# Optimization experiments

Measured on AMD Instinct MI355X. Metric: run time of the kernel, lower is better.

Reference implementation:

```python
import jax, jax.numpy as jnp
import numpy as np

B, N, DIM = 1, 2048, 2048
H, KVH = 32, 4                 # query heads, kv heads
D = DIM // H                   # head_dim = 64
REP = H // KVH                 # queries per kv = 8
KV_DIM = D * KVH               # 256


def _rope_tables(n, d, base=10000.0):
    inv = 1.0 / (base ** (np.arange(0, d, 2, dtype=np.float32) / d))
    t = np.arange(n, dtype=np.float32)
    freqs = np.outer(t, inv)                      # [n, d/2]
    emb = np.concatenate([freqs, freqs], axis=-1)  # [n, d]
    return jnp.asarray(np.cos(emb)), jnp.asarray(np.sin(emb))


def setup_inputs() -> dict:
    key = jax.random.key(0)
    ks = jax.random.split(key, 5)
    s = 0.02
    cos, sin = _rope_tables(N, D)
    return {
        "x": jax.random.normal(ks[0], (B, N, DIM), jnp.float32),
        "Wq": jax.random.normal(ks[1], (DIM, DIM), jnp.float32) * s,
        "Wk": jax.random.normal(ks[2], (KV_DIM, DIM), jnp.float32) * s,
        "Wv": jax.random.normal(ks[3], (KV_DIM, DIM), jnp.float32) * s,
        "Wo": jax.random.normal(ks[4], (DIM, DIM), jnp.float32) * s,
        "cos": cos,
        "sin": sin,
    }


def _rotate_half(t):
    d2 = t.shape[-1] // 2
    return jnp.concatenate([-t[..., d2:], t[..., :d2]], axis=-1)


def reference(x, Wq, Wk, Wv, Wo, cos, sin):
    b, n, _ = x.shape
    # projections (nn.Linear: x @ W.T)
    q = (x @ Wq.T).reshape(b, n, H, D).transpose(0, 2, 1, 3)     # b h n d
    k = (x @ Wk.T).reshape(b, n, KVH, D).transpose(0, 2, 1, 3)   # b g n d
    v = (x @ Wv.T).reshape(b, n, KVH, D).transpose(0, 2, 1, 3)
    # RoPE
    c = cos[None, None, :, :]
    s = sin[None, None, :, :]
    q = q * c + _rotate_half(q) * s
    k = k * c + _rotate_half(k) * s
    # expand KV heads (repeat_interleave over head dim)
    k = jnp.repeat(k, REP, axis=1)   # b h n d
    v = jnp.repeat(v, REP, axis=1)
    # causal attention with materialized scores (faithful to source)
    scale = 1.0 / jnp.sqrt(jnp.asarray(D, x.dtype))
    scores = jnp.einsum('bhld,bhsd->bhls', q, k) * scale
    causal = jnp.tril(jnp.ones((n, n), bool))
    scores = jnp.where(causal[None, None], scores, jnp.asarray(-jnp.inf, x.dtype))
    attn = jax.nn.softmax(scores, axis=-1)
    y = jnp.einsum('bhls,bhsd->bhld', attn, v)       # b h n d
    y = y.transpose(0, 2, 1, 3).reshape(b, n, DIM)   # b n (h d)
    return y @ Wo.T
```

## Files before the change

### kernel.cpp

```cpp
#include <hip/hip_runtime.h>

typedef unsigned short u16;
typedef __attribute__((ext_vector_type(8))) short short8;
typedef __attribute__((ext_vector_type(4))) float floatx4;

#define N_TOK 2048
#define DIM   2048
#define NH    32
#define NKVH  4
#define HD    64
#define KVD   256

__device__ __forceinline__ float bf2f(u16 u) {
  union { unsigned i; float f; } c; c.i = ((unsigned)u) << 16; return c.f;
}
__device__ __forceinline__ u16 f2bf(float f) {
  union { float f; unsigned i; } c; c.f = f;
  unsigned x = c.i;
  return (u16)((x + 0x7fffu + ((x >> 16) & 1u)) >> 16);
}

__device__ __forceinline__ void gload16(const u16* g, u16* l) {
#if defined(__has_builtin) && __has_builtin(__builtin_amdgcn_global_load_lds)
  __builtin_amdgcn_global_load_lds(
      (const __attribute__((address_space(1))) void*)g,
      (__attribute__((address_space(3))) void*)l, 16, 0, 0);
#else
  *(short8*)l = *(const short8*)g;
#endif
}

#define C_X  1048576
#define C_WQ 2097152
#define C_WK 2228224
#define C_WV 2359296
#define C_WO 3407872
__global__ __launch_bounds__(256) void cvt_all(const float* __restrict__ x,
                                               const float* __restrict__ wq,
                                               const float* __restrict__ wk,
                                               const float* __restrict__ wv,
                                               const float* __restrict__ wo,
                                               u16* __restrict__ dst) {
  int i = blockIdx.x * 256 + threadIdx.x;
  const float* src; int off;
  if      (i < C_X)  { src = x;  off = 0; }
  else if (i < C_WQ) { src = wq; off = C_X; }
  else if (i < C_WK) { src = wk; off = C_WQ; }
  else if (i < C_WV) { src = wv; off = C_WK; }
  else               { src = wo; off = C_WV; }
  float4 v = ((const float4*)src)[i - off];
  ushort4 o;
  o.x = f2bf(v.x); o.y = f2bf(v.y); o.z = f2bf(v.z); o.w = f2bf(v.w);
  ((ushort4*)dst)[i] = o;
}


__global__ __launch_bounds__(256) void gemm_qkv(const u16* __restrict__ A,
                                                const u16* __restrict__ Wq,
                                                const u16* __restrict__ Wk,
                                                const u16* __restrict__ Wv,
                                                const float* __restrict__ cs,
                                                const float* __restrict__ sn,
                                                u16* __restrict__ Qp,
                                                u16* __restrict__ Kp,
                                                u16* __restrict__ Vp) {
  __shared__ __align__(16) u16 As[64 * 32];
  __shared__ __align__(16) u16 Bs[128 * 32];
  const int tid  = threadIdx.x;
  const int lane = tid & 63;
  const int w    = tid >> 6;
  const int r    = lane & 15, q = lane >> 4;
  const int tm = blockIdx.x & 31;
  const int tn = blockIdx.x >> 5;
  const int wm = w & 1, wn = w >> 1;
  const int K = DIM;

  const u16* W; int wrow0;
  if (tn < 16)      { W = Wq; wrow0 = tn * 128; }
  else if (tn < 18) { W = Wk; wrow0 = (tn - 16) * 128; }
  else              { W = Wv; wrow0 = (tn - 18) * 128; }

  const int srow = tid >> 2;
  const int scol = (tid & 3) * 8;
  const u16* ga = A + (size_t)(tm * 64 + srow) * K + scol;
  const u16* gb = W + (size_t)(wrow0 + srow) * K + scol;
  u16* lA = &As[tid * 8];
  u16* lB = &Bs[tid * 8];

  floatx4 acc[2][4];
#pragma unroll
  for (int a = 0; a < 2; ++a)
#pragma unroll
    for (int b = 0; b < 4; ++b) acc[a][b] = (floatx4){0.f, 0.f, 0.f, 0.f};

  for (int k0 = 0; k0 < K; k0 += 32) {
    __syncthreads();
    gload16(ga + k0, lA);
    gload16(gb + k0, lB);
    gload16(gb + k0 + (size_t)64 * K, lB + 2048);
    __syncthreads();

    short8 af[2], bf[4];
#pragma unroll
    for (int mi = 0; mi < 2; ++mi)
      af[mi] = *(const short8*)&As[(wm * 32 + mi * 16 + r) * 32 + q * 8];
#pragma unroll
    for (int nj = 0; nj < 4; ++nj)
      bf[nj] = *(const short8*)&Bs[(wn * 64 + nj * 16 + r) * 32 + q * 8];
#pragma unroll
    for (int mi = 0; mi < 2; ++mi)
#pragma unroll
      for (int nj = 0; nj < 4; ++nj)
        acc[mi][nj] = __builtin_amdgcn_mfma_f32_16x16x32_bf16(af[mi], bf[nj], acc[mi][nj], 0, 0, 0);
  }

  if (tn < 18) {
    const int head = (tn < 16) ? (tn * 2 + wn) : ((tn - 16) * 2 + wn);
#pragma unroll
    for (int mi = 0; mi < 2; ++mi)
#pragma unroll
      for (int g = 0; g < 4; ++g) {
        int row = tm * 64 + wm * 32 + mi * 16 + 4 * q + g;
        const float* crow  = cs + (size_t)row * 64;
        const float* srow2 = sn + (size_t)row * 64;
#pragma unroll
        for (int nj = 0; nj < 2; ++nj) {
          int d = nj * 16 + r;
          float x0 = acc[mi][nj][g];
          float x1 = acc[mi][nj + 2][g];
          float o0 = x0 * crow[d]      - x1 * srow2[d];
          float o1 = x1 * crow[d + 32] + x0 * srow2[d + 32];
          int qq = d >> 3, j = d & 7;
          int lslot = (qq * 16 + (row & 15)) * 8 + j;
          if (tn < 16) {
            int sq = row >> 5, ii = (row >> 4) & 1;
            size_t base = ((size_t)(head * 64 + sq) * 4 + ii * 2) * 512 + lslot;
            Qp[base]       = f2bf(o0);
            Qp[base + 512] = f2bf(o1);
          } else {
            int kt = row >> 6, t = (row >> 4) & 3;
            size_t base = ((size_t)(head * 32 + kt) * 8 + t * 2) * 512 + lslot;
            Kp[base]       = f2bf(o0);
            Kp[base + 512] = f2bf(o1);
          }
        }
      }
  } else {
#pragma unroll
    for (int mi = 0; mi < 2; ++mi)
#pragma unroll
      for (int nj = 0; nj < 4; ++nj) {
        int col  = (tn - 18) * 128 + wn * 64 + nj * 16 + r;
        int kvh  = col >> 6;
        int t    = (col & 63) >> 4;
        int rr   = col & 15;
        int row0 = tm * 64 + wm * 32 + mi * 16 + 4 * q;
        int kt   = row0 >> 6;
        int wk   = row0 & 63;
        int s    = wk >> 5;
        int qq   = (wk & 31) >> 3;
        int j0   = wk & 7;
        uint2 pk;
        pk.x = (unsigned)f2bf(acc[mi][nj][0]) | ((unsigned)f2bf(acc[mi][nj][1]) << 16);
        pk.y = (unsigned)f2bf(acc[mi][nj][2]) | ((unsigned)f2bf(acc[mi][nj][3]) << 16);
        size_t idx = ((size_t)(kvh * 32 + kt) * 8 + s * 4 + t) * 512 + (qq * 16 + rr) * 8 + j0;
        *(uint2*)(Vp + idx) = pk;
      }
  }
}

__global__ __launch_bounds__(256) void gemm_out(const u16* __restrict__ A,
                                                const u16* __restrict__ W,
                                                float* __restrict__ C) {
  __shared__ __align__(16) u16 As[64 * 32];
  __shared__ __align__(16) u16 Bs[128 * 32];
  const int tid  = threadIdx.x;
  const int lane = tid & 63;
  const int w    = tid >> 6;
  const int r    = lane & 15, q = lane >> 4;
  const int tn = blockIdx.x & 15;
  const int tm = blockIdx.x >> 4;
  const int wm = w & 1, wn = w >> 1;
  const int K = DIM;

  const int srow = tid >> 2;
  const int scol = (tid & 3) * 8;
  const u16* ga = A + (size_t)(tm * 64 + srow) * K + scol;
  const u16* gb = W + (size_t)(tn * 128 + srow) * K + scol;
  u16* lA = &As[tid * 8];
  u16* lB = &Bs[tid * 8];

  floatx4 acc[2][4];
#pragma unroll
  for (int a = 0; a < 2; ++a)
#pragma unroll
    for (int b = 0; b < 4; ++b) acc[a][b] = (floatx4){0.f, 0.f, 0.f, 0.f};

  for (int k0 = 0; k0 < K; k0 += 32) {
    __syncthreads();
    gload16(ga + k0, lA);
    gload16(gb + k0, lB);
    gload16(gb + k0 + (size_t)64 * K, lB + 2048);
    __syncthreads();

    short8 af[2], bf[4];
#pragma unroll
    for (int mi = 0; mi < 2; ++mi)
      af[mi] = *(const short8*)&As[(wm * 32 + mi * 16 + r) * 32 + q * 8];
#pragma unroll
    for (int nj = 0; nj < 4; ++nj)
      bf[nj] = *(const short8*)&Bs[(wn * 64 + nj * 16 + r) * 32 + q * 8];
#pragma unroll
    for (int mi = 0; mi < 2; ++mi)
#pragma unroll
      for (int nj = 0; nj < 4; ++nj)
        acc[mi][nj] = __builtin_amdgcn_mfma_f32_16x16x32_bf16(af[mi], bf[nj], acc[mi][nj], 0, 0, 0);
  }

#pragma unroll
  for (int mi = 0; mi < 2; ++mi)
#pragma unroll
    for (int g = 0; g < 4; ++g) {
      int row = tm * 64 + wm * 32 + mi * 16 + 4 * q + g;
#pragma unroll
      for (int nj = 0; nj < 4; ++nj)
        C[(size_t)row * DIM + tn * 128 + wn * 64 + nj * 16 + r] = acc[mi][nj][g];
    }
}

__global__ __launch_bounds__(128, 2) void attn_mfma(const u16* __restrict__ Qp,
                                                    const u16* __restrict__ Kp,
                                                    const u16* __restrict__ Vp,
                                                    u16* __restrict__ Yb) {
  __shared__ __align__(16) u16 Pl[2][32][72];
  __shared__ float OcA[32][66];
  __shared__ float OcB[32][66];
  __shared__ float LcA[2][64], LcB[2][64];
  const int tid  = threadIdx.x;
  const int lane = tid & 63;
  const int w    = tid >> 6;
  const int r    = lane & 15;
  const int q    = lane >> 4;
  const int p    = blockIdx.x;
  const int h    = blockIdx.y;
  const int kvh  = h >> 3;
  const int jA   = 63 - p;
  const int jB   = p;
  const int baseqA = jA * 32, baseqB = jB * 32;
  const int tA = (jA >> 1) + 1, tB = (jB >> 1) + 1;
  const int ktmaxA = tA - 1, ktmaxB = tB - 1;

  short8 qfA[2][2], qfB[2][2];
#pragma unroll
  for (int i = 0; i < 2; ++i)
#pragma unroll
    for (int c = 0; c < 2; ++c) {
      qfA[i][c] = *(const short8*)(Qp + ((size_t)(h * 64 + jA) * 4 + i * 2 + c) * 512 + lane * 8);
      qfB[i][c] = *(const short8*)(Qp + ((size_t)(h * 64 + jB) * 4 + i * 2 + c) * 512 + lane * 8);
    }

  floatx4 OA[2][4], OB[2][4];
  float lsumA[2], lsumB[2];
#pragma unroll
  for (int i = 0; i < 2; ++i) {
    lsumA[i] = 0.f; lsumB[i] = 0.f;
#pragma unroll
    for (int t = 0; t < 4; ++t) {
      OA[i][t] = (floatx4){0.f, 0.f, 0.f, 0.f};
      OB[i][t] = (floatx4){0.f, 0.f, 0.f, 0.f};
    }
  }

  const u16* Kbase = Kp + (size_t)(kvh * 32) * 8 * 512;
  const u16* Vbase = Vp + (size_t)(kvh * 32) * 8 * 512;

  auto loadK = [&](int kt, short8 (&kf)[4][2]) {
    const u16* kb = Kbase + (size_t)kt * 8 * 512 + lane * 8;
#pragma unroll
    for (int t = 0; t < 4; ++t) {
      kf[t][0] = *(const short8*)(kb + (t * 2 + 0) * 512);
      kf[t][1] = *(const short8*)(kb + (t * 2 + 1) * 512);
    }
  };

  auto body = [&](int kt, int ktmax, int baseq,
                  short8 (&qf)[2][2], floatx4 (&O)[2][4], float (&lsum)[2],
                  short8 (&kc)[4][2], short8 (&kn)[4][2]) {
    short8 vb[2][4];
    {
      const u16* vbp = Vbase + (size_t)kt * 8 * 512 + lane * 8;
#pragma unroll
      for (int s = 0; s < 2; ++s)
#pragma unroll
        for (int t = 0; t < 4; ++t)
          vb[s][t] = *(const short8*)(vbp + (s * 4 + t) * 512);
    }

    loadK(kt + 2 <= ktmax ? kt + 2 : ktmax, kn);

    floatx4 ST[2][4];
#pragma unroll
    for (int i = 0; i < 2; ++i)
#pragma unroll
      for (int t = 0; t < 4; ++t) ST[i][t] = (floatx4){0.f, 0.f, 0.f, 0.f};
#pragma unroll
    for (int t = 0; t < 4; ++t)
#pragma unroll
      for (int i = 0; i < 2; ++i) {
        ST[i][t] = __builtin_amdgcn_mfma_f32_16x16x32_bf16(kc[t][0], qf[i][0], ST[i][t], 0, 0, 0);
        ST[i][t] = __builtin_amdgcn_mfma_f32_16x16x32_bf16(kc[t][1], qf[i][1], ST[i][t], 0, 0, 0);
      }

    if (kt == ktmax) {
#pragma unroll
      for (int i = 0; i < 2; ++i) {
        int qrow = baseq + 16 * i + r;
#pragma unroll
        for (int t = 0; t < 4; ++t) {
          int key = kt * 64 + 16 * t + 4 * q;
#pragma unroll
          for (int g = 0; g < 4; ++g)
            if (key + g > qrow) ST[i][t][g] = -1e30f;
        }
      }
    }

#pragma unroll
    for (int i = 0; i < 2; ++i)
#pragma unroll
      for (int t = 0; t < 4; ++t) {
        float p0 = __expf(0.125f * ST[i][t][0]);
        float p1 = __expf(0.125f * ST[i][t][1]);
        float p2 = __expf(0.125f * ST[i][t][2]);
        float p3 = __expf(0.125f * ST[i][t][3]);
        lsum[i] += (p0 + p1) + (p2 + p3);
        uint2 pk;
        pk.x = (unsigned)f2bf(p0) | ((unsigned)f2bf(p1) << 16);
        pk.y = (unsigned)f2bf(p2) | ((unsigned)f2bf(p3) << 16);
        *(uint2*)&Pl[w][16 * i + r][16 * t + 4 * q] = pk;
      }

#pragma unroll
    for (int s = 0; s < 2; ++s)
#pragma unroll
      for (int i = 0; i < 2; ++i) {
        short8 pa = *(const short8*)&Pl[w][16 * i + r][32 * s + 8 * q];
#pragma unroll
        for (int t = 0; t < 4; ++t)
          O[i][t] = __builtin_amdgcn_mfma_f32_16x16x32_bf16(pa, vb[s][t], O[i][t], 0, 0, 0);
      }
  };

  auto runloop = [&](int start, int ktmax, int baseq,
                     short8 (&qf)[2][2], floatx4 (&O)[2][4], float (&lsum)[2]) {
    if (start > ktmax) return;
    short8 kA[4][2], kB[4][2];
    loadK(start, kA);
    for (int kt = start; kt <= ktmax; kt += 4) {
      body(kt, ktmax, baseq, qf, O, lsum, kA, kB);
      if (kt + 2 <= ktmax) body(kt + 2, ktmax, baseq, qf, O, lsum, kB, kA);
    }
  };

  runloop(w, ktmaxA, baseqA, qfA, OA, lsumA);
  const int sB = (w + tA) & 1;
  runloop(sB, ktmaxB, baseqB, qfB, OB, lsumB);

  if (w == 1) {
#pragma unroll
    for (int i = 0; i < 2; ++i) {
#pragma unroll
      for (int t = 0; t < 4; ++t)
#pragma unroll
        for (int g = 0; g < 4; ++g)
          OcA[(i * 4 + t) * 4 + g][lane] = OA[i][t][g];
      LcA[i][lane] = lsumA[i];
    }
  } else {
#pragma unroll
    for (int i = 0; i < 2; ++i) {
#pragma unroll
      for (int t = 0; t < 4; ++t)
#pragma unroll
        for (int g = 0; g < 4; ++g)
          OcB[(i * 4 + t) * 4 + g][lane] = OB[i][t][g];
      LcB[i][lane] = lsumB[i];
    }
  }
  __syncthreads();

  auto finalize = [&](int baseq, floatx4 (&O)[2][4], float (&lsum)[2]) {
#pragma unroll
    for (int i = 0; i < 2; ++i) {
      lsum[i] += __shfl_xor(lsum[i], 16);
      lsum[i] += __shfl_xor(lsum[i], 32);
    }
#pragma unroll
    for (int i = 0; i < 2; ++i) {
      float inv[4];
#pragma unroll
      for (int g = 0; g < 4; ++g)
        inv[g] = 1.f / __shfl(lsum[i], 4 * q + g);
#pragma unroll
      for (int g = 0; g < 4; ++g) {
        u16* yp = Yb + (size_t)(baseq + 16 * i + 4 * q + g) * DIM + h * 64 + r;
        yp[0]  = f2bf(O[i][0][g] * inv[g]);
        yp[16] = f2bf(O[i][1][g] * inv[g]);
        yp[32] = f2bf(O[i][2][g] * inv[g]);
        yp[48] = f2bf(O[i][3][g] * inv[g]);
      }
    }
  };

  if (w == 0) {
#pragma unroll
    for (int i = 0; i < 2; ++i) {
#pragma unroll
      for (int t = 0; t < 4; ++t)
#pragma unroll
        for (int g = 0; g < 4; ++g)
          OA[i][t][g] += OcA[(i * 4 + t) * 4 + g][lane];
      lsumA[i] += LcA[i][lane];
    }
    finalize(baseqA, OA, lsumA);
  } else {
#pragma unroll
    for (int i = 0; i < 2; ++i) {
#pragma unroll
      for (int t = 0; t < 4; ++t)
#pragma unroll
        for (int g = 0; g < 4; ++g)
          OB[i][t][g] += OcB[(i * 4 + t) * 4 + g][lane];
      lsumB[i] += LcB[i][lane];
    }
    finalize(baseqB, OB, lsumB);
  }
}

extern "C" void kernel_launch(void* const* d_in, const int* in_sizes, int n_in,
                              void* d_out, int out_size, void* d_ws, size_t ws_size,
                              hipStream_t stream) {
  const float* x  = (const float*)d_in[0];
  const float* Wq = (const float*)d_in[1];
  const float* Wk = (const float*)d_in[2];
  const float* Wv = (const float*)d_in[3];
  const float* Wo = (const float*)d_in[4];
  const float* cs = (const float*)d_in[5];
  const float* sn = (const float*)d_in[6];

  u16* ws  = (u16*)d_ws;
  u16* xb  = ws;
  u16* Wqb = xb  + (size_t)N_TOK * DIM;
  u16* Wkb = Wqb + (size_t)DIM * DIM;
  u16* Wvb = Wkb + (size_t)KVD * DIM;
  u16* Wob = Wvb + (size_t)KVD * DIM;
  u16* Qp  = Wob + (size_t)DIM * DIM;
  u16* Kp  = Qp  + (size_t)N_TOK * DIM;
  u16* Vp  = Kp  + (size_t)N_TOK * KVD;
  u16* Yb  = Vp  + (size_t)N_TOK * KVD;

  cvt_all<<<dim3(13312), 256, 0, stream>>>(x, Wq, Wk, Wv, Wo, ws);

  gemm_qkv<<<dim3(640), 256, 0, stream>>>(xb, Wqb, Wkb, Wvb, cs, sn, Qp, Kp, Vp);

  attn_mfma<<<dim3(32, 32), 128, 0, stream>>>(Qp, Kp, Vp, Yb);

  gemm_out<<<dim3(512), 256, 0, stream>>>(Yb, Wob, (float*)d_out);
}
```

Baseline: 207.4 us.

## Double-buffer LDS tiles and XOR-swizzle layout in projection GEMMs

Both the QKV and output projection GEMMs now stage the next K-slice into a second LDS buffer while computing on the current one. This replaces two barriers per iteration with one and overlaps global-to-LDS loads with MFMA work. The LDS chunk position is XOR-swizzled by row to reduce bank conflicts on fragment reads. This doubles the LDS footprint per block, which may lower occupancy.

```diff
diff --git a/kernel.cpp b/kernel.cpp
--- a/kernel.cpp
+++ b/kernel.cpp
@@ -64,8 +64,8 @@
                                                 u16* __restrict__ Qp,
                                                 u16* __restrict__ Kp,
                                                 u16* __restrict__ Vp) {
-  __shared__ __align__(16) u16 As[64 * 32];
-  __shared__ __align__(16) u16 Bs[128 * 32];
+  __shared__ __align__(16) u16 As[2][64 * 32];
+  __shared__ __align__(16) u16 Bs[2][128 * 32];
   const int tid  = threadIdx.x;
   const int lane = tid & 63;
   const int w    = tid >> 6;
@@ -80,12 +80,13 @@
   else if (tn < 18) { W = Wk; wrow0 = (tn - 16) * 128; }
   else              { W = Wv; wrow0 = (tn - 18) * 128; }
 
-  const int srow = tid >> 2;
-  const int scol = (tid & 3) * 8;
+  const int srow   = tid >> 2;
+  const int schunk = (tid & 3) ^ ((srow >> 1) & 3);
+  const int scol   = schunk * 8;
   const u16* ga = A + (size_t)(tm * 64 + srow) * K + scol;
   const u16* gb = W + (size_t)(wrow0 + srow) * K + scol;
-  u16* lA = &As[tid * 8];
-  u16* lB = &Bs[tid * 8];
+
+  const int rsw = (q ^ ((r >> 1) & 3)) * 8;
 
   floatx4 acc[2][4];
 #pragma unroll
@@ -93,25 +94,33 @@
 #pragma unroll
     for (int b = 0; b < 4; ++b) acc[a][b] = (floatx4){0.f, 0.f, 0.f, 0.f};
 
+  auto stage = [&](int b, int k0) {
+    gload16(ga + k0, &As[b][tid * 8]);
+    gload16(gb + k0, &Bs[b][tid * 8]);
+    gload16(gb + k0 + (size_t)64 * K, &Bs[b][tid * 8 + 2048]);
+  };
+
+  stage(0, 0);
+  __syncthreads();
+  int cb = 0;
   for (int k0 = 0; k0 < K; k0 += 32) {
-    __syncthreads();
-    gload16(ga + k0, lA);
-    gload16(gb + k0, lB);
-    gload16(gb + k0 + (size_t)64 * K, lB + 2048);
-    __syncthreads();
+    if (k0 + 32 < K) stage(cb ^ 1, k0 + 32);
 
     short8 af[2], bf[4];
 #pragma unroll
     for (int mi = 0; mi < 2; ++mi)
-      af[mi] = *(const short8*)&As[(wm * 32 + mi * 16 + r) * 32 + q * 8];
+      af[mi] = *(const short8*)&As[cb][(wm * 32 + mi * 16 + r) * 32 + rsw];
 #pragma unroll
     for (int nj = 0; nj < 4; ++nj)
-      bf[nj] = *(const short8*)&Bs[(wn * 64 + nj * 16 + r) * 32 + q * 8];
+      bf[nj] = *(const short8*)&Bs[cb][(wn * 64 + nj * 16 + r) * 32 + rsw];
 #pragma unroll
     for (int mi = 0; mi < 2; ++mi)
 #pragma unroll
       for (int nj = 0; nj < 4; ++nj)
         acc[mi][nj] = __builtin_amdgcn_mfma_f32_16x16x32_bf16(af[mi], bf[nj], acc[mi][nj], 0, 0, 0);
+
+    __syncthreads();
+    cb ^= 1;
   }
 
   if (tn < 18) {
@@ -172,8 +181,8 @@
 __global__ __launch_bounds__(256) void gemm_out(const u16* __restrict__ A,
                                                 const u16* __restrict__ W,
                                                 float* __restrict__ C) {
-  __shared__ __align__(16) u16 As[64 * 32];
-  __shared__ __align__(16) u16 Bs[128 * 32];
+  __shared__ __align__(16) u16 As[2][64 * 32];
+  __shared__ __align__(16) u16 Bs[2][128 * 32];
   const int tid  = threadIdx.x;
   const int lane = tid & 63;
   const int w    = tid >> 6;
@@ -183,12 +192,13 @@
   const int wm = w & 1, wn = w >> 1;
   const int K = DIM;
 
-  const int srow = tid >> 2;
-  const int scol = (tid & 3) * 8;
+  const int srow   = tid >> 2;
+  const int schunk = (tid & 3) ^ ((srow >> 1) & 3);
+  const int scol   = schunk * 8;
   const u16* ga = A + (size_t)(tm * 64 + srow) * K + scol;
   const u16* gb = W + (size_t)(tn * 128 + srow) * K + scol;
-  u16* lA = &As[tid * 8];
-  u16* lB = &Bs[tid * 8];
+
+  const int rsw = (q ^ ((r >> 1) & 3)) * 8;
 
   floatx4 acc[2][4];
 #pragma unroll
@@ -196,25 +206,33 @@
 #pragma unroll
     for (int b = 0; b < 4; ++b) acc[a][b] = (floatx4){0.f, 0.f, 0.f, 0.f};
 
+  auto stage = [&](int b, int k0) {
+    gload16(ga + k0, &As[b][tid * 8]);
+    gload16(gb + k0, &Bs[b][tid * 8]);
+    gload16(gb + k0 + (size_t)64 * K, &Bs[b][tid * 8 + 2048]);
+  };
+
+  stage(0, 0);
+  __syncthreads();
+  int cb = 0;
   for (int k0 = 0; k0 < K; k0 += 32) {
-    __syncthreads();
-    gload16(ga + k0, lA);
-    gload16(gb + k0, lB);
-    gload16(gb + k0 + (size_t)64 * K, lB + 2048);
-    __syncthreads();
+    if (k0 + 32 < K) stage(cb ^ 1, k0 + 32);
 
     short8 af[2], bf[4];
 #pragma unroll
     for (int mi = 0; mi < 2; ++mi)
-      af[mi] = *(const short8*)&As[(wm * 32 + mi * 16 + r) * 32 + q * 8];
+      af[mi] = *(const short8*)&As[cb][(wm * 32 + mi * 16 + r) * 32 + rsw];
 #pragma unroll
     for (int nj = 0; nj < 4; ++nj)
-      bf[nj] = *(const short8*)&Bs[(wn * 64 + nj * 16 + r) * 32 + q * 8];
+      bf[nj] = *(const short8*)&Bs[cb][(wn * 64 + nj * 16 + r) * 32 + rsw];
 #pragma unroll
     for (int mi = 0; mi < 2; ++mi)
 #pragma unroll
       for (int nj = 0; nj < 4; ++nj)
         acc[mi][nj] = __builtin_amdgcn_mfma_f32_16x16x32_bf16(af[mi], bf[nj], acc[mi][nj], 0, 0, 0);
+
+    __syncthreads();
+    cb ^= 1;
   }
 
 #pragma unroll
```

Result: no change. 208.4 us (+0.5%).

## Use fragment-major LDS layout and K-step of 64 in projection GEMMs

Applied to the files above, without the earlier changes.

Both the QKV and output projection GEMMs now stage tiles in LDS in an MFMA-fragment-major order, so each lane reads its 16-byte fragment at a contiguous lane*8 offset instead of a row-strided address. The K step doubles from 32 to 64, halving the number of barrier pairs per tile and issuing twice as many MFMAs between syncs. LDS use per block doubles and global loads become 16-row gathers per wave, which may change coalescing. Local variables are also renamed to avoid shadowing.

```diff
diff --git a/kernel.cpp b/kernel.cpp
--- a/kernel.cpp
+++ b/kernel.cpp
@@ -64,8 +64,8 @@
                                                 u16* __restrict__ Qp,
                                                 u16* __restrict__ Kp,
                                                 u16* __restrict__ Vp) {
-  __shared__ __align__(16) u16 As[64 * 32];
-  __shared__ __align__(16) u16 Bs[128 * 32];
+  __shared__ __align__(16) u16 As[8 * 512];
+  __shared__ __align__(16) u16 Bs[16 * 512];
   const int tid  = threadIdx.x;
   const int lane = tid & 63;
   const int w    = tid >> 6;
@@ -80,12 +80,15 @@
   else if (tn < 18) { W = Wk; wrow0 = (tn - 16) * 128; }
   else              { W = Wv; wrow0 = (tn - 18) * 128; }
 
-  const int srow = tid >> 2;
-  const int scol = (tid & 3) * 8;
-  const u16* ga = A + (size_t)(tm * 64 + srow) * K + scol;
-  const u16* gb = W + (size_t)(wrow0 + srow) * K + scol;
-  u16* lA = &As[tid * 8];
-  u16* lB = &Bs[tid * 8];
+  const int chA0 = w, chA1 = w + 4;
+  const u16* gaP0 = A + (size_t)(tm * 64 + (chA0 >> 1) * 16 + r) * K + (chA0 & 1) * 32 + q * 8;
+  const u16* gaP1 = A + (size_t)(tm * 64 + (chA1 >> 1) * 16 + r) * K + (chA1 & 1) * 32 + q * 8;
+  const u16* gbP[4];
+#pragma unroll
+  for (int j = 0; j < 4; ++j) {
+    int ch = w + 4 * j;
+    gbP[j] = W + (size_t)(wrow0 + (ch >> 1) * 16 + r) * K + (ch & 1) * 32 + q * 8;
+  }
 
   floatx4 acc[2][4];
 #pragma unroll
@@ -93,25 +96,33 @@
 #pragma unroll
     for (int b = 0; b < 4; ++b) acc[a][b] = (floatx4){0.f, 0.f, 0.f, 0.f};
 
-  for (int k0 = 0; k0 < K; k0 += 32) {
+  for (int k0 = 0; k0 < K; k0 += 64) {
     __syncthreads();
-    gload16(ga + k0, lA);
-    gload16(gb + k0, lB);
-    gload16(gb + k0 + (size_t)64 * K, lB + 2048);
+    gload16(gaP0 + k0, &As[chA0 * 512 + lane * 8]);
+    gload16(gaP1 + k0, &As[chA1 * 512 + lane * 8]);
+#pragma unroll
+    for (int j = 0; j < 4; ++j)
+      gload16(gbP[j] + k0, &Bs[(w + 4 * j) * 512 + lane * 8]);
     __syncthreads();
 
-    short8 af[2], bf[4];
+    short8 af[2][2], bf[4][2];
 #pragma unroll
     for (int mi = 0; mi < 2; ++mi)
-      af[mi] = *(const short8*)&As[(wm * 32 + mi * 16 + r) * 32 + q * 8];
+#pragma unroll
+      for (int c = 0; c < 2; ++c)
+        af[mi][c] = *(const short8*)&As[((wm * 2 + mi) * 2 + c) * 512 + lane * 8];
 #pragma unroll
     for (int nj = 0; nj < 4; ++nj)
-      bf[nj] = *(const short8*)&Bs[(wn * 64 + nj * 16 + r) * 32 + q * 8];
-#pragma unroll
-    for (int mi = 0; mi < 2; ++mi)
-#pragma unroll
-      for (int nj = 0; nj < 4; ++nj)
-        acc[mi][nj] = __builtin_amdgcn_mfma_f32_16x16x32_bf16(af[mi], bf[nj], acc[mi][nj], 0, 0, 0);
+#pragma unroll
+      for (int c = 0; c < 2; ++c)
+        bf[nj][c] = *(const short8*)&Bs[((wn * 4 + nj) * 2 + c) * 512 + lane * 8];
+#pragma unroll
+    for (int c = 0; c < 2; ++c)
+#pragma unroll
+      for (int mi = 0; mi < 2; ++mi)
+#pragma unroll
+        for (int nj = 0; nj < 4; ++nj)
+          acc[mi][nj] = __builtin_amdgcn_mfma_f32_16x16x32_bf16(af[mi][c], bf[nj][c], acc[mi][nj], 0, 0, 0);
   }
 
   if (tn < 18) {
@@ -138,8 +149,8 @@
             Qp[base]       = f2bf(o0);
             Qp[base + 512] = f2bf(o1);
           } else {
-            int kt = row >> 6, t = (row >> 4) & 3;
-            size_t base = ((size_t)(head * 32 + kt) * 8 + t * 2) * 512 + lslot;
+            int kt2 = row >> 6, t = (row >> 4) & 3;
+            size_t base = ((size_t)(head * 32 + kt2) * 8 + t * 2) * 512 + lslot;
             Kp[base]       = f2bf(o0);
             Kp[base + 512] = f2bf(o1);
           }
@@ -155,7 +166,7 @@
         int t    = (col & 63) >> 4;
         int rr   = col & 15;
         int row0 = tm * 64 + wm * 32 + mi * 16 + 4 * q;
-        int kt   = row0 >> 6;
+        int kt2  = row0 >> 6;
         int wk   = row0 & 63;
         int s    = wk >> 5;
         int qq   = (wk & 31) >> 3;
@@ -163,7 +174,7 @@
         uint2 pk;
         pk.x = (unsigned)f2bf(acc[mi][nj][0]) | ((unsigned)f2bf(acc[mi][nj][1]) << 16);
         pk.y = (unsigned)f2bf(acc[mi][nj][2]) | ((unsigned)f2bf(acc[mi][nj][3]) << 16);
-        size_t idx = ((size_t)(kvh * 32 + kt) * 8 + s * 4 + t) * 512 + (qq * 16 + rr) * 8 + j0;
+        size_t idx = ((size_t)(kvh * 32 + kt2) * 8 + s * 4 + t) * 512 + (qq * 16 + rr) * 8 + j0;
         *(uint2*)(Vp + idx) = pk;
       }
   }
@@ -172,8 +183,8 @@
 __global__ __launch_bounds__(256) void gemm_out(const u16* __restrict__ A,
                                                 const u16* __restrict__ W,
                                                 float* __restrict__ C) {
-  __shared__ __align__(16) u16 As[64 * 32];
-  __shared__ __align__(16) u16 Bs[128 * 32];
+  __shared__ __align__(16) u16 As[8 * 512];
+  __shared__ __align__(16) u16 Bs[16 * 512];
   const int tid  = threadIdx.x;
   const int lane = tid & 63;
   const int w    = tid >> 6;
@@ -183,12 +194,15 @@
   const int wm = w & 1, wn = w >> 1;
   const int K = DIM;
 
-  const int srow = tid >> 2;
-  const int scol = (tid & 3) * 8;
-  const u16* ga = A + (size_t)(tm * 64 + srow) * K + scol;
-  const u16* gb = W + (size_t)(tn * 128 + srow) * K + scol;
-  u16* lA = &As[tid * 8];
-  u16* lB = &Bs[tid * 8];
+  const int chA0 = w, chA1 = w + 4;
+  const u16* gaP0 = A + (size_t)(tm * 64 + (chA0 >> 1) * 16 + r) * K + (chA0 & 1) * 32 + q * 8;
+  const u16* gaP1 = A + (size_t)(tm * 64 + (chA1 >> 1) * 16 + r) * K + (chA1 & 1) * 32 + q * 8;
+  const u16* gbP[4];
+#pragma unroll
+  for (int j = 0; j < 4; ++j) {
+    int ch = w + 4 * j;
+    gbP[j] = W + (size_t)(tn * 128 + (ch >> 1) * 16 + r) * K + (ch & 1) * 32 + q * 8;
+  }
 
   floatx4 acc[2][4];
 #pragma unroll
@@ -196,25 +210,33 @@
 #pragma unroll
     for (int b = 0; b < 4; ++b) acc[a][b] = (floatx4){0.f, 0.f, 0.f, 0.f};
 
-  for (int k0 = 0; k0 < K; k0 += 32) {
+  for (int k0 = 0; k0 < K; k0 += 64) {
     __syncthreads();
-    gload16(ga + k0, lA);
-    gload16(gb + k0, lB);
-    gload16(gb + k0 + (size_t)64 * K, lB + 2048);
+    gload16(gaP0 + k0, &As[chA0 * 512 + lane * 8]);
+    gload16(gaP1 + k0, &As[chA1 * 512 + lane * 8]);
+#pragma unroll
+    for (int j = 0; j < 4; ++j)
+      gload16(gbP[j] + k0, &Bs[(w + 4 * j) * 512 + lane * 8]);
     __syncthreads();
 
-    short8 af[2], bf[4];
+    short8 af[2][2], bf[4][2];
 #pragma unroll
     for (int mi = 0; mi < 2; ++mi)
-      af[mi] = *(const short8*)&As[(wm * 32 + mi * 16 + r) * 32 + q * 8];
+#pragma unroll
+      for (int c = 0; c < 2; ++c)
+        af[mi][c] = *(const short8*)&As[((wm * 2 + mi) * 2 + c) * 512 + lane * 8];
 #pragma unroll
     for (int nj = 0; nj < 4; ++nj)
-      bf[nj] = *(const short8*)&Bs[(wn * 64 + nj * 16 + r) * 32 + q * 8];
-#pragma unroll
-    for (int mi = 0; mi < 2; ++mi)
-#pragma unroll
-      for (int nj = 0; nj < 4; ++nj)
-        acc[mi][nj] = __builtin_amdgcn_mfma_f32_16x16x32_bf16(af[mi], bf[nj], acc[mi][nj], 0, 0, 0);
+#pragma unroll
+      for (int c = 0; c < 2; ++c)
+        bf[nj][c] = *(const short8*)&Bs[((wn * 4 + nj) * 2 + c) * 512 + lane * 8];
+#pragma unroll
+    for (int c = 0; c < 2; ++c)
+#pragma unroll
+      for (int mi = 0; mi < 2; ++mi)
+#pragma unroll
+        for (int nj = 0; nj < 4; ++nj)
+          acc[mi][nj] = __builtin_amdgcn_mfma_f32_16x16x32_bf16(af[mi][c], bf[nj][c], acc[mi][nj], 0, 0, 0);
   }
 
 #pragma unroll
```

New measurement: 248.4 us. +19.8%, slower.
